# Optimization experiments

Hardware: AMD Instinct MI355X
Metric: run time of the kernel (lower is better)

## Reference

```python
import jax, jax.numpy as jnp
import numpy as np

CH_IN = 256
CH_OUT = 32


def setup_inputs() -> dict:
    key = jax.random.key(0)
    ks = jax.random.split(key, 7)
    b, c, H, W = 4, CH_IN, 64, 64
    x = jax.random.normal(ks[0], (b, c, H, W), dtype=jnp.float32)
    # 1x1 conv weights (out, in) and biases, small init like torch default
    sc_in = 1.0 / np.sqrt(CH_IN)
    Wf = jax.random.uniform(ks[1], (CH_OUT, CH_IN), jnp.float32, -sc_in, sc_in)
    bf = jax.random.uniform(ks[2], (CH_OUT,), jnp.float32, -sc_in, sc_in)
    Wg = jax.random.uniform(ks[3], (CH_OUT, CH_IN), jnp.float32, -sc_in, sc_in)
    bg = jax.random.uniform(ks[4], (CH_OUT,), jnp.float32, -sc_in, sc_in)
    Wh = jax.random.uniform(ks[5], (CH_IN, CH_IN), jnp.float32, -sc_in, sc_in)
    bh = jax.random.uniform(ks[6], (CH_IN,), jnp.float32, -sc_in, sc_in)
    return {"x": x, "Wf": Wf, "bf": bf, "Wg": Wg, "bg": bg, "Wh": Wh, "bh": bh}


def reference(x, Wf, bf, Wg, bg, Wh, bh):
    b, c, H, W = x.shape
    xf = x.reshape(b, c, H * W)                      # [b, c, N]
    # 1x1 convs == per-pixel linear projections
    f = jnp.einsum('oc,bcn->bon', Wf, xf) + bf[None, :, None]   # [b, ch_out, N]
    g = jnp.einsum('oc,bcn->bon', Wg, xf) + bg[None, :, None]   # [b, ch_out, N]
    h = jnp.einsum('oc,bcn->bon', Wh, xf) + bh[None, :, None]   # [b, ch_in, N]
    # s[b, i, j] = sum_o f[b,o,i] * g[b,o,j]
    s = jnp.einsum('boi,boj->bij', f, g)             # [b, N, N]
    # torch softmax over dim=1 (the i axis)
    beta = jax.nn.softmax(s, axis=1)                 # [b, N, N]
    # o = h @ beta : [b, c, N] x [b, N, N] -> [b, c, N]
    o = jnp.einsum('bcn,bnm->bcm', h, beta)
    return o.reshape(b, c, H, W)
```

## Files before the change

kernel.cpp:

```cpp
#include <hip/hip_runtime.h>
#include <hip/hip_bf16.h>
#include <math.h>

#define BATCH 4
#define CIN   256
#define DQK   32
#define NPIX  4096
#define MTOT  320

typedef __attribute__((ext_vector_type(4))) float f32x4;
typedef __attribute__((ext_vector_type(8))) short bf16x8;
typedef __attribute__((ext_vector_type(4))) unsigned int u32x4;

__device__ __forceinline__ unsigned short f2bf(float f) {
  unsigned u = __builtin_bit_cast(unsigned, f);
  u += 0x7FFFu + ((u >> 16) & 1u);
  return (unsigned short)(u >> 16);
}
__device__ __forceinline__ unsigned pk2(float a, float b) {
  return (unsigned)f2bf(a) | ((unsigned)f2bf(b) << 16);
}
__device__ __forceinline__ void barrier_lds() {
  asm volatile("s_waitcnt lgkmcnt(0)" ::: "memory");
  __builtin_amdgcn_s_barrier();
  asm volatile("" ::: "memory");
}

__global__ void wcvt(const float* __restrict__ Wh, const float* __restrict__ Wf,
                     const float* __restrict__ Wg,
                     const float* __restrict__ bh, const float* __restrict__ bf,
                     const float* __restrict__ bg,
                     unsigned short* __restrict__ Wb, float* __restrict__ bcat) {
  const int r = blockIdx.x;
  const int c = threadIdx.x;
  const float* src = (r < 256) ? &Wh[r * CIN] : (r < 288) ? &Wf[(r - 256) * CIN] : &Wg[(r - 288) * CIN];
  Wb[r * CIN + c] = f2bf(src[c]);
  if (c == 0)
    bcat[r] = (r < 256) ? bh[r] : (r < 288) ? bf[r - 256] : bg[r - 288];
}

#define XPAD 4
__launch_bounds__(512, 1)
__global__ void proj_all(const float* __restrict__ x, const unsigned short* __restrict__ Wb,
                         const float* __restrict__ bcat,
                         unsigned short* __restrict__ F, unsigned short* __restrict__ G,
                         unsigned short* __restrict__ H) {
  __shared__ unsigned short Xs[64 * (CIN + XPAD)];

  const int bid = blockIdx.x;
  const int b = bid >> 6;
  const int n0 = (bid & 63) << 6;
  const int t = threadIdx.x;
  const int lane = t & 63;
  const int w = t >> 6;

  const float* __restrict__ xb = x + (size_t)b * CIN * NPIX + n0;
#pragma unroll
  for (int p = 0; p < 16; ++p) {
    const int k = p * 16 + w * 2;
    const float a0 = xb[(size_t)k * NPIX + lane];
    const float a1 = xb[(size_t)(k + 1) * NPIX + lane];
    const unsigned pk = (unsigned)f2bf(a0) | ((unsigned)f2bf(a1) << 16);
    *(unsigned*)((char*)Xs + lane * (CIN + XPAD) * 2 + k * 2) = pk;
  }
  __syncthreads();

  const int l16 = lane & 15, lhi = lane >> 4;
  const int wm = w >> 1;
  const int wn = w & 1;

  const f32x4 fzero = {0.f, 0.f, 0.f, 0.f};
  f32x4 acc[5][2];
#pragma unroll
  for (int i = 0; i < 5; ++i)
#pragma unroll
    for (int j = 0; j < 2; ++j) acc[i][j] = fzero;

#pragma unroll
  for (int ks = 0; ks < 8; ++ks) {
    bf16x8 bx[2];
#pragma unroll
    for (int j = 0; j < 2; ++j)
      bx[j] = *(const bf16x8*)&Xs[(wn * 32 + j * 16 + l16) * (CIN + XPAD) + ks * 32 + lhi * 8];
#pragma unroll
    for (int i = 0; i < 5; ++i) {
      const bf16x8 aw = *(const bf16x8*)(Wb + (size_t)(wm * 80 + i * 16 + l16) * CIN + ks * 32 + lhi * 8);
#pragma unroll
      for (int j = 0; j < 2; ++j)
        acc[i][j] = __builtin_amdgcn_mfma_f32_16x16x32_bf16(aw, bx[j], acc[i][j], 0, 0, 0);
    }
  }

#pragma unroll
  for (int i = 0; i < 5; ++i) {
    const int MT = wm * 5 + i;
    const int m0 = MT * 16;
    const f32x4 bias = *(const f32x4*)&bcat[m0 + lhi * 4];
#pragma unroll
    for (int j = 0; j < 2; ++j) {
      const int n = n0 + wn * 32 + j * 16 + l16;
      f32x4 v = acc[i][j];
      v.x += bias.x; v.y += bias.y; v.z += bias.z; v.w += bias.w;
      if (MT < 16) {
        const int c0 = m0 + lhi * 4;
        unsigned short* dst = H + ((size_t)b * CIN + c0) * NPIX + n;
        dst[0 * NPIX] = f2bf(v.x);
        dst[1 * NPIX] = f2bf(v.y);
        dst[2 * NPIX] = f2bf(v.z);
        dst[3 * NPIX] = f2bf(v.w);
      } else {
        unsigned short* dst = (MT < 18) ? F : G;
        const int d0 = ((MT - 16) & 1) * 16 + lhi * 4;
        uint2 pk;
        pk.x = (unsigned)f2bf(v.x) | ((unsigned)f2bf(v.y) << 16);
        pk.y = (unsigned)f2bf(v.z) | ((unsigned)f2bf(v.w) << 16);
        *(uint2*)(dst + ((size_t)b * NPIX + n) * DQK + d0) = pk;
      }
    }
  }
}

#define QT   128
#define BNK  64
#define KEYS 2048
#define NTILE (KEYS / BNK)

__launch_bounds__(512, 2)
__global__ void attn_split(const unsigned short* __restrict__ F,
                           const unsigned short* __restrict__ G,
                           const unsigned short* __restrict__ H,
                           unsigned short* __restrict__ Ap, float* __restrict__ Lp) {
  __shared__ unsigned short Kl[2][64][36];
  __shared__ unsigned short Vl[2][256][72];
  __shared__ unsigned short Pl[2][64][72];

  const int bid = blockIdx.x;
  const int split = bid & 1;
  const int qt = (bid >> 1) & 31;
  const int b = bid >> 6;
  const int t = threadIdx.x;
  const int lane = t & 63, w = t >> 6;
  const int l16 = lane & 15, lhi = lane >> 4;
  const int mg = w >> 2, cs = w & 3;

  const unsigned short* Fb = F + (size_t)b * NPIX * DQK;
  const unsigned short* Gb = G + (size_t)b * NPIX * DQK;
  const unsigned short* Hb = H + (size_t)b * CIN * NPIX;
  const int nb0 = split * KEYS;
  const int q0 = qt * QT + mg * 64;

  const f32x4 fzero = {0.f, 0.f, 0.f, 0.f};

  bf16x8 qf[4];
#pragma unroll
  for (int mt = 0; mt < 4; ++mt)
    qf[mt] = *(const bf16x8*)(Gb + (size_t)(q0 + mt * 16 + l16) * DQK + lhi * 8);

  f32x4 acc[4][4];
#pragma unroll
  for (int ct = 0; ct < 4; ++ct)
#pragma unroll
    for (int mt = 0; mt < 4; ++mt) acc[ct][mt] = fzero;
  float Lacc[4] = {0.f, 0.f, 0.f, 0.f};

  const int vrow = t >> 3, vslot = t & 7;
  const int krow = t >> 2, kslot = t & 3;

  u32x4 vr0[4], vr1[4], kr0, kr1;

#define STAGE_LOAD(VR, KR, TILE_) do {                                                   \
    const int nb_ = nb0 + (TILE_) * BNK;                                                 \
    _Pragma("unroll")                                                                    \
    for (int i_ = 0; i_ < 4; ++i_)                                                       \
      VR[i_] = *(const u32x4*)(Hb + (size_t)(i_ * 64 + vrow) * NPIX + nb_ + vslot * 8);  \
    if (t < 256) KR = *(const u32x4*)(Fb + (size_t)(nb_ + krow) * DQK + kslot * 8);      \
  } while (0)

#define STAGE_STORE(VR, KR, BUF) do {                                                    \
    _Pragma("unroll")                                                                    \
    for (int i_ = 0; i_ < 4; ++i_)                                                       \
      *(u32x4*)&Vl[BUF][i_ * 64 + vrow][vslot * 8] = VR[i_];                             \
    if (t < 256) *(u32x4*)&Kl[BUF][krow][kslot * 8] = KR;                                \
  } while (0)

#define COMPUTE(BUF) do {                                                                \
    const bf16x8 kf = *(const bf16x8*)&Kl[BUF][cs * 16 + l16][lhi * 8];                  \
    f32x4 s_[4];                                                                         \
    _Pragma("unroll")                                                                    \
    for (int mt = 0; mt < 4; ++mt)                                                       \
      s_[mt] = __builtin_amdgcn_mfma_f32_16x16x32_bf16(kf, qf[mt], fzero, 0, 0, 0);      \
    _Pragma("unroll")                                                                    \
    for (int mt = 0; mt < 4; ++mt) {                                                     \
      const float p0 = __expf(s_[mt][0]), p1 = __expf(s_[mt][1]);                        \
      const float p2 = __expf(s_[mt][2]), p3 = __expf(s_[mt][3]);                        \
      Lacc[mt] += (p0 + p1) + (p2 + p3);                                                 \
      uint2 pk; pk.x = pk2(p0, p1); pk.y = pk2(p2, p3);                                  \
      *(uint2*)&Pl[mg][mt * 16 + l16][cs * 16 + lhi * 4] = pk;                           \
    }                                                                                    \
    barrier_lds();                                                                       \
    _Pragma("unroll")                                                                    \
    for (int kk = 0; kk < 2; ++kk) {                                                     \
      bf16x8 pf[4];                                                                      \
      _Pragma("unroll")                                                                  \
      for (int mt = 0; mt < 4; ++mt)                                                     \
        pf[mt] = *(const bf16x8*)&Pl[mg][mt * 16 + l16][kk * 32 + lhi * 8];              \
      _Pragma("unroll")                                                                  \
      for (int ct = 0; ct < 4; ++ct) {                                                   \
        const bf16x8 vf = *(const bf16x8*)&Vl[BUF][cs * 64 + ct * 16 + l16][kk * 32 + lhi * 8]; \
        _Pragma("unroll")                                                                \
        for (int mt = 0; mt < 4; ++mt)                                                   \
          acc[ct][mt] = __builtin_amdgcn_mfma_f32_16x16x32_bf16(vf, pf[mt], acc[ct][mt], 0, 0, 0); \
      }                                                                                  \
    }                                                                                    \
    barrier_lds();                                                                       \
  } while (0)

  STAGE_LOAD(vr0, kr0, 0);
  STAGE_STORE(vr0, kr0, 0);
  STAGE_LOAD(vr1, kr1, 1);
  barrier_lds();

  for (int tt = 0; tt < NTILE; tt += 2) {
    if (tt + 1 < NTILE) STAGE_STORE(vr1, kr1, 1);
    if (tt + 2 < NTILE) STAGE_LOAD(vr0, kr0, tt + 2);
    COMPUTE(0);
    if (tt + 2 < NTILE) STAGE_STORE(vr0, kr0, 0);
    if (tt + 3 < NTILE) STAGE_LOAD(vr1, kr1, tt + 3);
    COMPUTE(1);
  }

#pragma unroll
  for (int mt = 0; mt < 4; ++mt) {
    float L = Lacc[mt];
    L += __shfl_xor(L, 16, 64);
    L += __shfl_xor(L, 32, 64);
    if (lhi == 0)
      Lp[((size_t)split * 4 + cs) * (4 * NPIX) + (size_t)b * NPIX + q0 + mt * 16 + l16] = L;
  }
#pragma unroll
  for (int ct = 0; ct < 4; ++ct)
#pragma unroll
    for (int mt = 0; mt < 4; ++mt) {
      const int c = cs * 64 + ct * 16 + lhi * 4;
      const int q = q0 + mt * 16 + l16;
      unsigned short* dst = Ap + (((size_t)split * 4 + b) * CIN + c) * NPIX + q;
#pragma unroll
      for (int v = 0; v < 4; ++v) dst[(size_t)v * NPIX] = f2bf(acc[ct][mt][v]);
    }
#undef STAGE_LOAD
#undef STAGE_STORE
#undef COMPUTE
}

__global__ void combineL(const float* __restrict__ Lp, float* __restrict__ Linv) {
  const int idx = blockIdx.x * 256 + threadIdx.x;
  float s = 0.f;
#pragma unroll
  for (int i = 0; i < 8; ++i) s += Lp[(size_t)i * (4 * NPIX) + idx];
  Linv[idx] = 1.f / s;
}

__global__ void combine(const unsigned short* __restrict__ Ap, const float* __restrict__ Linv,
                        float* __restrict__ out) {
  const size_t base = ((size_t)blockIdx.x * 256 + threadIdx.x) * 8;
  const int b = (int)(base / ((size_t)CIN * NPIX));
  const int q = (int)(base % NPIX);
  const u32x4 a0 = *(const u32x4*)(Ap + base);
  const u32x4 a1 = *(const u32x4*)(Ap + (size_t)4 * CIN * NPIX + base);
  const float* lv = &Linv[(size_t)b * NPIX + q];
  float r[8];
#pragma unroll
  for (int i = 0; i < 4; ++i) {
    const float x0 = __builtin_bit_cast(float, (a0[i] & 0xFFFFu) << 16) +
                     __builtin_bit_cast(float, (a1[i] & 0xFFFFu) << 16);
    const float x1 = __builtin_bit_cast(float, (a0[i] & 0xFFFF0000u)) +
                     __builtin_bit_cast(float, (a1[i] & 0xFFFF0000u));
    r[2 * i] = x0 * lv[2 * i];
    r[2 * i + 1] = x1 * lv[2 * i + 1];
  }
  *(f32x4*)&out[base] = *(f32x4*)&r[0];
  *(f32x4*)&out[base + 4] = *(f32x4*)&r[4];
}

#define BN 32
__launch_bounds__(512, 2)
__global__ void attn_kernel(const unsigned short* __restrict__ F,
                            const unsigned short* __restrict__ G,
                            const unsigned short* __restrict__ H,
                            float* __restrict__ out) {
  __shared__ unsigned short Klds[32 * 40];
  __shared__ unsigned short Vlds[256 * 40];
  __shared__ unsigned short Plds[8][32 * 40];

  const int bid = blockIdx.x;
  const int b = bid >> 6;
  const int t = threadIdx.x;
  const int lane = t & 63;
  const int w = t >> 6;
  const int l16 = lane & 15;
  const int lhi = lane >> 4;
  const int m0 = ((bid & 63) << 6) + ((w >> 2) << 5);
  const int c0 = (w & 3) << 6;

  const f32x4 fzero = {0.f, 0.f, 0.f, 0.f};

  bf16x8 qf[2];
#pragma unroll
  for (int mt = 0; mt < 2; ++mt)
    qf[mt] = *(const bf16x8*)(G + ((size_t)b * NPIX + m0 + mt * 16 + l16) * DQK + lhi * 8);

  f32x4 acc[4][2];
#pragma unroll
  for (int ct = 0; ct < 4; ++ct)
#pragma unroll
    for (int mt = 0; mt < 2; ++mt) acc[ct][mt] = fzero;
  float Mr[2] = {-INFINITY, -INFINITY};
  float Lr[2] = {0.f, 0.f};

  const unsigned short* Fb = F + (size_t)b * NPIX * DQK;
  const unsigned short* Hb = H + (size_t)b * CIN * NPIX;
  unsigned short* Pw = &Plds[w][0];

  for (int n0 = 0; n0 < NPIX; n0 += BN) {
    __syncthreads();
    if (t < 128) {
      const int nr = t >> 2, sl = t & 3;
      *(u32x4*)&Klds[nr * 40 + sl * 8] = *(const u32x4*)(Fb + (size_t)(n0 + nr) * DQK + sl * 8);
    }
#pragma unroll
    for (int i = 0; i < 2; ++i) {
      const int q = t + i * 512;
      const int cr = q >> 2, sl = q & 3;
      *(u32x4*)&Vlds[cr * 40 + sl * 8] = *(const u32x4*)(Hb + (size_t)cr * NPIX + n0 + sl * 8);
    }
    __syncthreads();

    bf16x8 kf[2];
#pragma unroll
    for (int nts = 0; nts < 2; ++nts)
      kf[nts] = *(const bf16x8*)&Klds[(nts * 16 + l16) * 40 + lhi * 8];
    f32x4 s[2][2];
#pragma unroll
    for (int mt = 0; mt < 2; ++mt)
#pragma unroll
      for (int nts = 0; nts < 2; ++nts)
        s[mt][nts] = __builtin_amdgcn_mfma_f32_16x16x32_bf16(kf[nts], qf[mt], fzero, 0, 0, 0);

#pragma unroll
    for (int mt = 0; mt < 2; ++mt) {
      float tmax = s[mt][0][0];
#pragma unroll
      for (int v = 1; v < 4; ++v) tmax = fmaxf(tmax, s[mt][0][v]);
#pragma unroll
      for (int v = 0; v < 4; ++v) tmax = fmaxf(tmax, s[mt][1][v]);
      tmax = fmaxf(tmax, __shfl_xor(tmax, 16, 64));
      tmax = fmaxf(tmax, __shfl_xor(tmax, 32, 64));
      const float newM = fmaxf(Mr[mt], tmax);
      const float rescale = __expf(Mr[mt] - newM);
      Mr[mt] = newM;
      float p[2][4];
      float psum = 0.f;
#pragma unroll
      for (int nts = 0; nts < 2; ++nts)
#pragma unroll
        for (int v = 0; v < 4; ++v) {
          p[nts][v] = __expf(s[mt][nts][v] - newM);
          psum += p[nts][v];
        }
      psum += __shfl_xor(psum, 16, 64);
      psum += __shfl_xor(psum, 32, 64);
      Lr[mt] = Lr[mt] * rescale + psum;
#pragma unroll
      for (int ct = 0; ct < 4; ++ct) acc[ct][mt] *= rescale;
#pragma unroll
      for (int nts = 0; nts < 2; ++nts) {
        uint2 pkv;
        pkv.x = (unsigned)f2bf(p[nts][0]) | ((unsigned)f2bf(p[nts][1]) << 16);
        pkv.y = (unsigned)f2bf(p[nts][2]) | ((unsigned)f2bf(p[nts][3]) << 16);
        *(uint2*)&Pw[(mt * 16 + l16) * 40 + nts * 16 + lhi * 4] = pkv;
      }
    }
    asm volatile("" ::: "memory");

    bf16x8 pf[2];
#pragma unroll
    for (int mt = 0; mt < 2; ++mt)
      pf[mt] = *(const bf16x8*)&Pw[(mt * 16 + l16) * 40 + lhi * 8];
#pragma unroll
    for (int ct = 0; ct < 4; ++ct) {
      const bf16x8 vf = *(const bf16x8*)&Vlds[(c0 + ct * 16 + l16) * 40 + lhi * 8];
#pragma unroll
      for (int mt = 0; mt < 2; ++mt)
        acc[ct][mt] = __builtin_amdgcn_mfma_f32_16x16x32_bf16(vf, pf[mt], acc[ct][mt], 0, 0, 0);
    }
  }

#pragma unroll
  for (int mt = 0; mt < 2; ++mt) {
    const float invL = 1.f / Lr[mt];
    const int m = m0 + mt * 16 + l16;
#pragma unroll
    for (int ct = 0; ct < 4; ++ct)
#pragma unroll
      for (int v = 0; v < 4; ++v) {
        const int c = c0 + ct * 16 + lhi * 4 + v;
        out[((size_t)b * CIN + c) * NPIX + m] = acc[ct][mt][v] * invL;
      }
  }
}

extern "C" void kernel_launch(void* const* d_in, const int* in_sizes, int n_in,
                              void* d_out, int out_size, void* d_ws, size_t ws_size,
                              hipStream_t stream) {
  (void)in_sizes; (void)n_in; (void)out_size;
  const float* x  = (const float*)d_in[0];
  const float* Wf = (const float*)d_in[1];
  const float* bf = (const float*)d_in[2];
  const float* Wg = (const float*)d_in[3];
  const float* bg = (const float*)d_in[4];
  const float* Wh = (const float*)d_in[5];
  const float* bh = (const float*)d_in[6];
  float* out = (float*)d_out;

  unsigned short* Fw = (unsigned short*)d_ws;
  unsigned short* Gw = Fw + (size_t)BATCH * NPIX * DQK;
  unsigned short* Hw = Gw + (size_t)BATCH * NPIX * DQK;
  unsigned short* Wb = Hw + (size_t)BATCH * CIN * NPIX;
  float* bcat = (float*)(Wb + (size_t)MTOT * CIN);
  unsigned short* Apart = (unsigned short*)(bcat + MTOT);
  float* Lpart = (float*)(Apart + (size_t)2 * BATCH * CIN * NPIX);
  float* Linv  = Lpart + (size_t)8 * BATCH * NPIX;
  const size_t NEED = (size_t)((char*)(Linv + (size_t)BATCH * NPIX) - (char*)d_ws);

  hipLaunchKernelGGL(wcvt, dim3(MTOT), dim3(256), 0, stream, Wh, Wf, Wg, bh, bf, bg, Wb, bcat);
  hipLaunchKernelGGL(proj_all, dim3(BATCH * 64), dim3(512), 0, stream, x, Wb, bcat, Fw, Gw, Hw);

  if (ws_size >= NEED) {
    hipLaunchKernelGGL(attn_split, dim3(BATCH * 32 * 2), dim3(512), 0, stream, Fw, Gw, Hw, Apart, Lpart);
    hipLaunchKernelGGL(combineL, dim3(BATCH * NPIX / 256), dim3(256), 0, stream, Lpart, Linv);
    hipLaunchKernelGGL(combine, dim3((size_t)BATCH * CIN * NPIX / 8 / 256), dim3(256), 0, stream, Apart, Linv, out);
  } else {
    hipLaunchKernelGGL(attn_kernel, dim3(BATCH * 64), dim3(512), 0, stream, Fw, Gw, Hw, out);
  }
}
```

Before: 88.11 us.

## Load V fragments directly from global into registers, drop V LDS staging

Restructures attn_split so each 256-thread block handles 64 queries. Each wave loads its V (H) MFMA fragments straight from global memory into registers instead of staging them through shared memory, which removes the V LDS buffer and one barrier per tile. The P buffer is now double-buffered, and s_setprio raises wave priority around the MFMA section. The grid is doubled and blocks are reordered so batch and split index come from the low bits. This cuts LDS traffic and synchronisation, but each block now re-reads V from global/L2 with less sharing across query tiles.

```diff
diff --git a/kernel.cpp b/kernel.cpp
--- a/kernel.cpp
+++ b/kernel.cpp
@@ -120,34 +120,31 @@
   }
 }
 
-#define QT   128
 #define BNK  64
 #define KEYS 2048
 #define NTILE (KEYS / BNK)
 
-__launch_bounds__(512, 2)
+__launch_bounds__(256, 2)
 __global__ void attn_split(const unsigned short* __restrict__ F,
                            const unsigned short* __restrict__ G,
                            const unsigned short* __restrict__ H,
                            unsigned short* __restrict__ Ap, float* __restrict__ Lp) {
   __shared__ unsigned short Kl[2][64][36];
-  __shared__ unsigned short Vl[2][256][72];
   __shared__ unsigned short Pl[2][64][72];
 
   const int bid = blockIdx.x;
+  const int b = (bid & 7) >> 1;
   const int split = bid & 1;
-  const int qt = (bid >> 1) & 31;
-  const int b = bid >> 6;
+  const int qt = bid >> 3;
   const int t = threadIdx.x;
-  const int lane = t & 63, w = t >> 6;
+  const int lane = t & 63, cs = t >> 6;
   const int l16 = lane & 15, lhi = lane >> 4;
-  const int mg = w >> 2, cs = w & 3;
 
   const unsigned short* Fb = F + (size_t)b * NPIX * DQK;
   const unsigned short* Gb = G + (size_t)b * NPIX * DQK;
   const unsigned short* Hb = H + (size_t)b * CIN * NPIX;
   const int nb0 = split * KEYS;
-  const int q0 = qt * QT + mg * 64;
+  const int q0 = qt * 64;
 
   const f32x4 fzero = {0.f, 0.f, 0.f, 0.f};
 
@@ -163,70 +160,62 @@
     for (int mt = 0; mt < 4; ++mt) acc[ct][mt] = fzero;
   float Lacc[4] = {0.f, 0.f, 0.f, 0.f};
 
-  const int vrow = t >> 3, vslot = t & 7;
   const int krow = t >> 2, kslot = t & 3;
-
-  u32x4 vr0[4], vr1[4], kr0, kr1;
-
-#define STAGE_LOAD(VR, KR, TILE_) do {                                                   \
-    const int nb_ = nb0 + (TILE_) * BNK;                                                 \
-    _Pragma("unroll")                                                                    \
-    for (int i_ = 0; i_ < 4; ++i_)                                                       \
-      VR[i_] = *(const u32x4*)(Hb + (size_t)(i_ * 64 + vrow) * NPIX + nb_ + vslot * 8);  \
-    if (t < 256) KR = *(const u32x4*)(Fb + (size_t)(nb_ + krow) * DQK + kslot * 8);      \
-  } while (0)
-
-#define STAGE_STORE(VR, KR, BUF) do {                                                    \
-    _Pragma("unroll")                                                                    \
-    for (int i_ = 0; i_ < 4; ++i_)                                                       \
-      *(u32x4*)&Vl[BUF][i_ * 64 + vrow][vslot * 8] = VR[i_];                             \
-    if (t < 256) *(u32x4*)&Kl[BUF][krow][kslot * 8] = KR;                                \
-  } while (0)
-
-#define COMPUTE(BUF) do {                                                                \
-    const bf16x8 kf = *(const bf16x8*)&Kl[BUF][cs * 16 + l16][lhi * 8];                  \
-    f32x4 s_[4];                                                                         \
-    _Pragma("unroll")                                                                    \
-    for (int mt = 0; mt < 4; ++mt)                                                       \
-      s_[mt] = __builtin_amdgcn_mfma_f32_16x16x32_bf16(kf, qf[mt], fzero, 0, 0, 0);      \
-    _Pragma("unroll")                                                                    \
-    for (int mt = 0; mt < 4; ++mt) {                                                     \
-      const float p0 = __expf(s_[mt][0]), p1 = __expf(s_[mt][1]);                        \
-      const float p2 = __expf(s_[mt][2]), p3 = __expf(s_[mt][3]);                        \
-      Lacc[mt] += (p0 + p1) + (p2 + p3);                                                 \
-      uint2 pk; pk.x = pk2(p0, p1); pk.y = pk2(p2, p3);                                  \
-      *(uint2*)&Pl[mg][mt * 16 + l16][cs * 16 + lhi * 4] = pk;                           \
-    }                                                                                    \
-    barrier_lds();                                                                       \
-    _Pragma("unroll")                                                                    \
-    for (int kk = 0; kk < 2; ++kk) {                                                     \
-      bf16x8 pf[4];                                                                      \
-      _Pragma("unroll")                                                                  \
-      for (int mt = 0; mt < 4; ++mt)                                                     \
-        pf[mt] = *(const bf16x8*)&Pl[mg][mt * 16 + l16][kk * 32 + lhi * 8];              \
-      _Pragma("unroll")                                                                  \
-      for (int ct = 0; ct < 4; ++ct) {                                                   \
-        const bf16x8 vf = *(const bf16x8*)&Vl[BUF][cs * 64 + ct * 16 + l16][kk * 32 + lhi * 8]; \
-        _Pragma("unroll")                                                                \
-        for (int mt = 0; mt < 4; ++mt)                                                   \
-          acc[ct][mt] = __builtin_amdgcn_mfma_f32_16x16x32_bf16(vf, pf[mt], acc[ct][mt], 0, 0, 0); \
-      }                                                                                  \
-    }                                                                                    \
-    barrier_lds();                                                                       \
-  } while (0)
-
-  STAGE_LOAD(vr0, kr0, 0);
-  STAGE_STORE(vr0, kr0, 0);
-  STAGE_LOAD(vr1, kr1, 1);
+  const unsigned short* Kg = Fb + ((size_t)(nb0 + krow)) * DQK + kslot * 8;
+  const unsigned short* vp[4];
+#pragma unroll
+  for (int ct = 0; ct < 4; ++ct)
+    vp[ct] = Hb + (size_t)(cs * 64 + ct * 16 + l16) * NPIX + nb0 + lhi * 8;
+
+  u32x4 kr;
+  kr = *(const u32x4*)Kg;
+  *(u32x4*)&Kl[0][krow][kslot * 8] = kr;
+  kr = *(const u32x4*)(Kg + 1 * BNK * DQK);
   barrier_lds();
 
-  for (int tt = 0; tt < NTILE; tt += 2) {
-    if (tt + 1 < NTILE) STAGE_STORE(vr1, kr1, 1);
-    if (tt + 2 < NTILE) STAGE_LOAD(vr0, kr0, tt + 2);
-    COMPUTE(0);
-    if (tt + 2 < NTILE) STAGE_STORE(vr0, kr0, 0);
-    if (tt + 3 < NTILE) STAGE_LOAD(vr1, kr1, tt + 3);
-    COMPUTE(1);
+  for (int tt = 0; tt < NTILE; ++tt) {
+    const int buf = tt & 1;
+    u32x4 vr[8];
+#pragma unroll
+    for (int ct = 0; ct < 4; ++ct)
+#pragma unroll
+      for (int kk = 0; kk < 2; ++kk)
+        vr[ct * 2 + kk] = *(const u32x4*)(vp[ct] + (size_t)tt * BNK + kk * 32);
+    if (tt + 1 < NTILE) *(u32x4*)&Kl[buf ^ 1][krow][kslot * 8] = kr;
+    if (tt + 2 < NTILE) kr = *(const u32x4*)(Kg + (size_t)(tt + 2) * BNK * DQK);
+
+    const bf16x8 kf = *(const bf16x8*)&Kl[buf][cs * 16 + l16][lhi * 8];
+    f32x4 s_[4];
+#pragma unroll
+    for (int mt = 0; mt < 4; ++mt)
+      s_[mt] = __builtin_amdgcn_mfma_f32_16x16x32_bf16(kf, qf[mt], fzero, 0, 0, 0);
+
+#pragma unroll
+    for (int mt = 0; mt < 4; ++mt) {
+      const float p0 = __expf(s_[mt][0]), p1 = __expf(s_[mt][1]);
+      const float p2 = __expf(s_[mt][2]), p3 = __expf(s_[mt][3]);
+      Lacc[mt] += (p0 + p1) + (p2 + p3);
+      uint2 pk; pk.x = pk2(p0, p1); pk.y = pk2(p2, p3);
+      *(uint2*)&Pl[buf][mt * 16 + l16][cs * 16 + lhi * 4] = pk;
+    }
+    barrier_lds();
+
+    __builtin_amdgcn_s_setprio(1);
+#pragma unroll
+    for (int kk = 0; kk < 2; ++kk) {
+      bf16x8 pf[4];
+#pragma unroll
+      for (int mt = 0; mt < 4; ++mt)
+        pf[mt] = *(const bf16x8*)&Pl[buf][mt * 16 + l16][kk * 32 + lhi * 8];
+#pragma unroll
+      for (int ct = 0; ct < 4; ++ct) {
+        const bf16x8 vf = __builtin_bit_cast(bf16x8, vr[ct * 2 + kk]);
+#pragma unroll
+        for (int mt = 0; mt < 4; ++mt)
+          acc[ct][mt] = __builtin_amdgcn_mfma_f32_16x16x32_bf16(vf, pf[mt], acc[ct][mt], 0, 0, 0);
+      }
+    }
+    __builtin_amdgcn_s_setprio(0);
   }
 
 #pragma unroll
@@ -247,9 +236,6 @@
 #pragma unroll
       for (int v = 0; v < 4; ++v) dst[(size_t)v * NPIX] = f2bf(acc[ct][mt][v]);
     }
-#undef STAGE_LOAD
-#undef STAGE_STORE
-#undef COMPUTE
 }
 
 __global__ void combineL(const float* __restrict__ Lp, float* __restrict__ Linv) {
@@ -436,7 +422,7 @@
   hipLaunchKernelGGL(proj_all, dim3(BATCH * 64), dim3(512), 0, stream, x, Wb, bcat, Fw, Gw, Hw);
 
   if (ws_size >= NEED) {
-    hipLaunchKernelGGL(attn_split, dim3(BATCH * 32 * 2), dim3(512), 0, stream, Fw, Gw, Hw, Apart, Lpart);
+    hipLaunchKernelGGL(attn_split, dim3(BATCH * 64 * 2), dim3(256), 0, stream, Fw, Gw, Hw, Apart, Lpart);
     hipLaunchKernelGGL(combineL, dim3(BATCH * NPIX / 256), dim3(256), 0, stream, Lpart, Linv);
     hipLaunchKernelGGL(combine, dim3((size_t)BATCH * CIN * NPIX / 8 / 256), dim3(256), 0, stream, Apart, Linv, out);
   } else {
```

New measurement: 99.10 us. 12.5% more time.
